# Kernel optimization log

Hardware: AMD Instinct MI355X
Metric: run time of the kernel (lower is better)

The kernel has to match this reference:

```python
import jax, jax.numpy as jnp
import numpy as np

STRIDE = 2
PAD = 1
K = 4
OUT_PAD = 0


def setup_inputs() -> dict:
    key = jax.random.key(0)
    k1, k2, k3, k4 = jax.random.split(key, 4)
    x = jax.random.normal(k1, (16, 64, 128, 128), dtype=jnp.float32)
    # torch ConvTranspose2d weight layout: [in_channels, out_channels, kH, kW]
    w = jax.random.normal(k2, (64, 32, 4, 4), dtype=jnp.float32) * 0.05
    conv_b = jax.random.normal(k3, (32,), dtype=jnp.float32) * 0.05
    bias = jax.random.normal(k4, (1, 1, 1, 1), dtype=jnp.float32)
    return {"x": x, "w": w, "conv_b": conv_b, "bias": bias}


def conv_transpose2d(x, w, conv_b):
    # Equivalent of torch ConvTranspose2d(k=4, s=2, p=1, op=0):
    # dilate input by stride, pad by k-1-p (+op on trailing side), conv with flipped kernel.
    lo = K - 1 - PAD
    hi = K - 1 - PAD + OUT_PAD
    w_oihw = jnp.flip(w, axis=(2, 3)).transpose(1, 0, 2, 3)  # [Cout, Cin, kH, kW]
    y = jax.lax.conv_general_dilated(
        x, w_oihw,
        window_strides=(1, 1),
        padding=((lo, hi), (lo, hi)),
        lhs_dilation=(STRIDE, STRIDE),
        dimension_numbers=("NCHW", "OIHW", "NCHW"),
    )
    return y + conv_b[None, :, None, None]


def reference(x, w, conv_b, bias):
    y = conv_transpose2d(x, w, conv_b)          # [N, Cout, H', W']
    y = jnp.min(y, axis=1, keepdims=True)       # channel-min -> [N,1,H',W']
    y = jnp.sum(y, axis=2, keepdims=True)       # height-sum  -> [N,1,1,W']
    # kernel uses tanh-based GELU approximation
    return jax.nn.gelu(y, approximate=True) + bias
```

## Files before the change

kernel.cpp:

```cpp
#include <hip/hip_runtime.h>
#include <math.h>

typedef __attribute__((ext_vector_type(8))) short short8;
typedef __attribute__((ext_vector_type(16))) float f32x16;
typedef __attribute__((ext_vector_type(2))) unsigned uintx2;

#define XS_STRIDE 72
#define RING 6

__device__ __forceinline__ short f2bf(float f) {
    union { float f; unsigned u; } v; v.f = f;
    unsigned r = (v.u + 0x7FFFu + ((v.u >> 16) & 1u)) >> 16;
    return (short)r;
}

__device__ __forceinline__ unsigned cvt_pk_bf16(float lo, float hi) {
    unsigned r;
    asm("v_cvt_pk_bf16_f32 %0, %1, %2" : "=v"(r) : "v"(lo), "v"(hi));
    return r;
}

__global__ void prep(const float* __restrict__ w, short* __restrict__ wfrag,
                     float* __restrict__ acc) {
    if (blockIdx.x >= 128) {
        #pragma unroll
        for (int i = 0; i < 16; ++i) acc[i * 256 + threadIdx.x] = 0.f;
        return;
    }
    int idx = blockIdx.x * 256 + threadIdx.x;
    int j    = idx & 7;
    int lane = (idx >> 3) & 63;
    int q    = (idx >> 9) & 15;
    int p    = idx >> 13;
    int co = lane & 31, hf = lane >> 5;
    int ci = (q & 3) * 16 + hf * 8 + j;
    int tq = q >> 2, a = tq >> 1, b = tq & 1;
    int ph = p >> 1, pw = p & 1;
    int kh = 2 * a + 1 - ph, kw = 2 * b + 1 - pw;
    wfrag[idx] = f2bf(w[((ci * 32 + co) * 4 + kh) * 4 + kw]);
}

__global__ __launch_bounds__(256, 3) void convt_mfma(
    const float* __restrict__ x, const short* __restrict__ wfrag,
    const float* __restrict__ conv_b, float* __restrict__ acc4096)
{
    __shared__ short xs[RING][34][XS_STRIDE];
    __shared__ float minbuf[2][2][4][32];

    const int blk = blockIdx.x;
    const int jq = blk & 3;
    const int st = (blk >> 2) & 15;
    const int n  = blk >> 6;
    const int t  = threadIdx.x;
    const int i0 = st * 8;

    const int wv = t >> 6, lane = t & 63;
    const int ph = wv >> 1, pw = wv & 1;
    const int ln = lane & 31, half = lane >> 5;

    short8 af[16];
    {
        const short8* wf = (const short8*)(wfrag + wv * 8192);
        #pragma unroll
        for (int q = 0; q < 16; ++q) af[q] = wf[q * 64 + lane];
    }
    float cb[16];
    #pragma unroll
    for (int reg = 0; reg < 16; ++reg)
        cb[reg] = conv_b[(reg & 3) + 8 * (reg >> 2) + 4 * half];

    const float* xn = x + (size_t)n * 64 * 128 * 128;

    const int col  = t & 31;
    const int cib  = (t >> 5) * 8;
    const int gcol = jq * 32 + col;
    const int hrow = t >> 7, hside = (t >> 6) & 1, hci = t & 63;
    const int hgc  = jq * 32 + (hside ? 32 : -1);
    const int sl_base = i0 % RING;

    #pragma unroll
    for (int r = 0; r < 4; ++r) {
        int gi = i0 - 1 + r;
        int slot = sl_base + r; if (slot >= RING) slot -= RING;
        bool rowok = (unsigned)gi < 128u;
        int gic = rowok ? gi : 0;
        const float* px = xn + ((size_t)cib * 128 + gic) * 128 + gcol;
        float v[8];
        #pragma unroll
        for (int c = 0; c < 8; ++c) v[c] = rowok ? px[c * 16384] : 0.f;
        uintx2 u0, u1;
        u0.x = cvt_pk_bf16(v[0], v[1]); u0.y = cvt_pk_bf16(v[2], v[3]);
        u1.x = cvt_pk_bf16(v[4], v[5]); u1.y = cvt_pk_bf16(v[6], v[7]);
        *(uintx2*)&xs[slot][col + 1][cib]     = u0;
        *(uintx2*)&xs[slot][col + 1][cib + 4] = u1;
    }
    {
        int r = t >> 6, ci = t & 63, gi = i0 - 1 + r;
        int slot = sl_base + r; if (slot >= RING) slot -= RING;
        #pragma unroll
        for (int side = 0; side < 2; ++side) {
            int gc = jq * 32 + (side ? 32 : -1);
            float v = ((unsigned)gi < 128u && (unsigned)gc < 128u)
                    ? xn[((size_t)ci * 128 + gi) * 128 + gc] : 0.f;
            xs[slot][side ? 33 : 0][ci] = f2bf(v);
        }
    }

    float pf[2][8]; float pfh;
    auto issue = [&](int r0) {
        #pragma unroll
        for (int r2 = 0; r2 < 2; ++r2) {
            int gi = r0 + r2;
            bool rowok = (unsigned)gi < 128u;
            int gic = rowok ? gi : 0;
            const float* px = xn + ((size_t)cib * 128 + gic) * 128 + gcol;
            #pragma unroll
            for (int c = 0; c < 8; ++c) pf[r2][c] = rowok ? px[c * 16384] : 0.f;
        }
        int gi = r0 + hrow;
        pfh = ((unsigned)gi < 128u && (unsigned)hgc < 128u)
            ? xn[((size_t)hci * 128 + gi) * 128 + hgc] : 0.f;
    };
    issue(i0 + 3);

    __syncthreads();

    float osum = 0.f;
    const int rpr = t >> 6;
    const int pw2 = (t >> 5) & 1;
    const int jl  = t & 31;

    int rbase = sl_base;
    #pragma unroll
    for (int k = 0; k < 4; ++k) {
        const int kb = k & 1;
        int s0 = rbase + ph; if (s0 >= RING) s0 -= RING;
        int s1 = s0 + 1;     if (s1 >= RING) s1 -= RING;
        int s2 = s1 + 1;     if (s2 >= RING) s2 -= RING;

        f32x16 acc0, acc1;
        #pragma unroll
        for (int reg = 0; reg < 16; ++reg) { acc0[reg] = cb[reg]; acc1[reg] = cb[reg]; }
        __builtin_amdgcn_s_setprio(1);
        #pragma unroll
        for (int b = 0; b < 2; ++b) {
            int colp = ln + (pw - b) + 1;
            const short* p0 = &xs[s0][colp][half * 8];
            const short* p1 = &xs[s1][colp][half * 8];
            const short* p2 = &xs[s2][colp][half * 8];
            #pragma unroll
            for (int c = 0; c < 4; ++c) {
                short8 Fs = *(const short8*)(p1 + c * 16);
                acc0 = __builtin_amdgcn_mfma_f32_32x32x16_bf16(af[4*b+c],   Fs, acc0, 0, 0, 0);
                acc1 = __builtin_amdgcn_mfma_f32_32x32x16_bf16(af[8+4*b+c], Fs, acc1, 0, 0, 0);
                short8 F0 = *(const short8*)(p0 + c * 16);
                acc0 = __builtin_amdgcn_mfma_f32_32x32x16_bf16(af[8+4*b+c], F0, acc0, 0, 0, 0);
                short8 F2 = *(const short8*)(p2 + c * 16);
                acc1 = __builtin_amdgcn_mfma_f32_32x32x16_bf16(af[4*b+c],   F2, acc1, 0, 0, 0);
            }
        }
        __builtin_amdgcn_s_setprio(0);

        float mn0 = acc0[0], mn1 = acc1[0];
        #pragma unroll
        for (int reg = 1; reg < 16; ++reg) {
            mn0 = fminf(mn0, acc0[reg]); mn1 = fminf(mn1, acc1[reg]);
        }
        mn0 = fminf(mn0, __shfl_xor(mn0, 32, 64));
        mn1 = fminf(mn1, __shfl_xor(mn1, 32, 64));
        if (half == 0) {
            minbuf[kb][0][wv][ln] = mn0;
            minbuf[kb][1][wv][ln] = mn1;
        }

        if (k < 3) {
            int ws0 = rbase + 4; if (ws0 >= RING) ws0 -= RING;
            int ws1 = ws0 + 1;   if (ws1 >= RING) ws1 -= RING;
            #pragma unroll
            for (int r2 = 0; r2 < 2; ++r2) {
                int slot = r2 ? ws1 : ws0;
                uintx2 u0, u1;
                u0.x = cvt_pk_bf16(pf[r2][0], pf[r2][1]);
                u0.y = cvt_pk_bf16(pf[r2][2], pf[r2][3]);
                u1.x = cvt_pk_bf16(pf[r2][4], pf[r2][5]);
                u1.y = cvt_pk_bf16(pf[r2][6], pf[r2][7]);
                *(uintx2*)&xs[slot][col + 1][cib]     = u0;
                *(uintx2*)&xs[slot][col + 1][cib + 4] = u1;
            }
            xs[hrow ? ws1 : ws0][hside ? 33 : 0][hci] = f2bf(pfh);
            if (k < 2) issue(i0 + 2 * k + 5);
        }
        __syncthreads();
        if (t < 128)
            osum += minbuf[kb][rpr][pw2][jl] + minbuf[kb][rpr][2 + pw2][jl];
        rbase += 2; if (rbase >= RING) rbase -= RING;
    }

    float* sbuf = &minbuf[0][0][0][0];
    if (t < 128) sbuf[t] = osum;
    __syncthreads();
    if (t < 64) {
        float v = sbuf[t] + sbuf[t + 64];
        int ow = ((jq * 32 + (t & 31)) << 1) | ((t >> 5) & 1);
        atomicAdd(&acc4096[n * 256 + ow], v);
    }
}

__global__ void finalize(const float* __restrict__ acc4096,
                         const float* __restrict__ bias, float* __restrict__ out)
{
    int idx = blockIdx.x * 256 + threadIdx.x;
    float s = acc4096[idx];
    float u = 0.7978845608028654f * (s + 0.044715f * s * s * s);
    out[idx] = 0.5f * s * (1.f + tanhf(u)) + bias[0];
}

extern "C" void kernel_launch(void* const* d_in, const int* in_sizes, int n_in,
                              void* d_out, int out_size, void* d_ws, size_t ws_size,
                              hipStream_t stream) {
    const float* x      = (const float*)d_in[0];
    const float* w      = (const float*)d_in[1];
    const float* conv_b = (const float*)d_in[2];
    const float* bias   = (const float*)d_in[3];
    float* out = (float*)d_out;

    float* acc   = (float*)d_ws;
    short* wfrag = (short*)((char*)d_ws + 16384);

    hipLaunchKernelGGL(prep, dim3(129), dim3(256), 0, stream, w, wfrag, acc);
    hipLaunchKernelGGL(convt_mfma, dim3(16 * 16 * 4), dim3(256), 0, stream,
                       x, wfrag, conv_b, acc);
    hipLaunchKernelGGL(finalize, dim3(16), dim3(256), 0, stream,
                       acc, bias, out);
}
```

Measured before the change: 123.8 us.

## Use lighter barriers, remap block order, replace atomics with partial sums, tree-reduce min

Replaces __syncthreads with a barrier that waits only on LDS counters, so outstanding global prefetch loads are not drained at each sync. Block indices are remapped so that consecutive blocks are spread across XCD-friendly groups. The atomicAdd accumulation is replaced by per-strip partial writes that the finalize kernel sums, which also removes the zeroing of the accumulator in prep. The min over accumulator registers is restructured as a tree to shorten the dependency chain. The lighter barrier relies on the compiler correctly inserting vmcnt waits before prefetched registers are used.

```diff
diff --git a/kernel.cpp b/kernel.cpp
--- a/kernel.cpp
+++ b/kernel.cpp
@@ -20,13 +20,14 @@
     return r;
 }
 
-__global__ void prep(const float* __restrict__ w, short* __restrict__ wfrag,
-                     float* __restrict__ acc) {
-    if (blockIdx.x >= 128) {
-        #pragma unroll
-        for (int i = 0; i < 16; ++i) acc[i * 256 + threadIdx.x] = 0.f;
-        return;
-    }
+__device__ __forceinline__ void bar_nodrain() {
+    __builtin_amdgcn_sched_barrier(0);
+    asm volatile("s_waitcnt lgkmcnt(0)" ::: "memory");
+    __builtin_amdgcn_s_barrier();
+    __builtin_amdgcn_sched_barrier(0);
+}
+
+__global__ void prep(const float* __restrict__ w, short* __restrict__ wfrag) {
     int idx = blockIdx.x * 256 + threadIdx.x;
     int j    = idx & 7;
     int lane = (idx >> 3) & 63;
@@ -42,12 +43,12 @@
 
 __global__ __launch_bounds__(256, 3) void convt_mfma(
     const float* __restrict__ x, const short* __restrict__ wfrag,
-    const float* __restrict__ conv_b, float* __restrict__ acc4096)
+    const float* __restrict__ conv_b, float* __restrict__ partials)
 {
     __shared__ short xs[RING][34][XS_STRIDE];
     __shared__ float minbuf[2][2][4][32];
 
-    const int blk = blockIdx.x;
+    int blk = ((blockIdx.x & 7) << 7) | (blockIdx.x >> 3);
     const int jq = blk & 3;
     const int st = (blk >> 2) & 15;
     const int n  = blk >> 6;
@@ -123,7 +124,7 @@
     };
     issue(i0 + 3);
 
-    __syncthreads();
+    bar_nodrain();
 
     float osum = 0.f;
     const int rpr = t >> 6;
@@ -161,10 +162,18 @@
         }
         __builtin_amdgcn_s_setprio(0);
 
-        float mn0 = acc0[0], mn1 = acc1[0];
-        #pragma unroll
-        for (int reg = 1; reg < 16; ++reg) {
-            mn0 = fminf(mn0, acc0[reg]); mn1 = fminf(mn1, acc1[reg]);
+        float mn0, mn1;
+        {
+            float a = fminf(fminf(acc0[0], acc0[1]), fminf(acc0[2], acc0[3]));
+            float b2 = fminf(fminf(acc0[4], acc0[5]), fminf(acc0[6], acc0[7]));
+            float c = fminf(fminf(acc0[8], acc0[9]), fminf(acc0[10], acc0[11]));
+            float d = fminf(fminf(acc0[12], acc0[13]), fminf(acc0[14], acc0[15]));
+            mn0 = fminf(fminf(a, b2), fminf(c, d));
+            a = fminf(fminf(acc1[0], acc1[1]), fminf(acc1[2], acc1[3]));
+            b2 = fminf(fminf(acc1[4], acc1[5]), fminf(acc1[6], acc1[7]));
+            c = fminf(fminf(acc1[8], acc1[9]), fminf(acc1[10], acc1[11]));
+            d = fminf(fminf(acc1[12], acc1[13]), fminf(acc1[14], acc1[15]));
+            mn1 = fminf(fminf(a, b2), fminf(c, d));
         }
         mn0 = fminf(mn0, __shfl_xor(mn0, 32, 64));
         mn1 = fminf(mn1, __shfl_xor(mn1, 32, 64));
@@ -190,7 +199,7 @@
             xs[hrow ? ws1 : ws0][hside ? 33 : 0][hci] = f2bf(pfh);
             if (k < 2) issue(i0 + 2 * k + 5);
         }
-        __syncthreads();
+        bar_nodrain();
         if (t < 128)
             osum += minbuf[kb][rpr][pw2][jl] + minbuf[kb][rpr][2 + pw2][jl];
         rbase += 2; if (rbase >= RING) rbase -= RING;
@@ -198,19 +207,21 @@
 
     float* sbuf = &minbuf[0][0][0][0];
     if (t < 128) sbuf[t] = osum;
-    __syncthreads();
+    bar_nodrain();
     if (t < 64) {
         float v = sbuf[t] + sbuf[t + 64];
         int ow = ((jq * 32 + (t & 31)) << 1) | ((t >> 5) & 1);
-        atomicAdd(&acc4096[n * 256 + ow], v);
-    }
-}
-
-__global__ void finalize(const float* __restrict__ acc4096,
+        partials[(size_t)st * 4096 + n * 256 + ow] = v;
+    }
+}
+
+__global__ void finalize(const float* __restrict__ partials,
                          const float* __restrict__ bias, float* __restrict__ out)
 {
     int idx = blockIdx.x * 256 + threadIdx.x;
-    float s = acc4096[idx];
+    float s = 0.f;
+    #pragma unroll
+    for (int st = 0; st < 16; ++st) s += partials[st * 4096 + idx];
     float u = 0.7978845608028654f * (s + 0.044715f * s * s * s);
     out[idx] = 0.5f * s * (1.f + tanhf(u)) + bias[0];
 }
@@ -224,12 +235,12 @@
     const float* bias   = (const float*)d_in[3];
     float* out = (float*)d_out;
 
-    float* acc   = (float*)d_ws;
-    short* wfrag = (short*)((char*)d_ws + 16384);
-
-    hipLaunchKernelGGL(prep, dim3(129), dim3(256), 0, stream, w, wfrag, acc);
+    short* wfrag    = (short*)d_ws;
+    float* partials = (float*)((char*)d_ws + 65536);
+
+    hipLaunchKernelGGL(prep, dim3(128), dim3(256), 0, stream, w, wfrag);
     hipLaunchKernelGGL(convt_mfma, dim3(16 * 16 * 4), dim3(256), 0, stream,
-                       x, wfrag, conv_b, acc);
+                       x, wfrag, conv_b, partials);
     hipLaunchKernelGGL(finalize, dim3(16), dim3(256), 0, stream,
-                       acc, bias, out);
-}
+                       partials, bias, out);
+}
```

Measured after the change: 129.4 us. 1.04x slower.
